# Performance work log

Hardware: AMD Instinct MI355X
Metric: run time of the kernel (lower is better)

The kernel has to match this reference:

```python
import jax, jax.numpy as jnp
import numpy as np

K = 5        # kernel_size per pseudo-dim
DIM = 2      # pseudo-coordinate dimensionality
K2 = K * K   # total kernel weight matrices
N_NODES = 50000


def spline_basis(edge_attr):
    """Open B-spline basis, degree=1, dim=2. Returns basis [E,4], weight_index [E,4]."""
    v = edge_attr * (K - 1)                      # [E,2], pseudo in [0,1]
    lo = jnp.floor(v)
    frac = v - lo                                # [E,2]
    lo = lo.astype(jnp.int32)
    fac = jnp.stack([1.0 - frac, frac], axis=-1)                 # [E,2,2] (dim, bit)
    idx = jnp.clip(lo[..., None] + jnp.arange(2), 0, K - 1)      # [E,2,2]
    b0 = jnp.array([0, 1, 0, 1])  # bit for dim 0, per spline term
    b1 = jnp.array([0, 0, 1, 1])  # bit for dim 1
    basis = fac[:, 0, b0] * fac[:, 1, b1]        # [E,4]
    wi = idx[:, 0, b0] * K + idx[:, 1, b1]       # [E,4] flat kernel index
    return basis, wi


def spline_conv(x, src, dst, basis, wi, W, root, bias, n_nodes):
    """SplineConv with mean aggregation, root weight and bias.
    x:[N,Fin] W:[K2,Fin,Fout] root:[Fin,Fout] bias:[Fout]"""
    E = src.shape[0]
    K2_, Fin, Fout = W.shape
    # scatter the 4 sparse basis values into a dense per-edge kernel-coeff matrix [E,K2]
    coeff = jnp.zeros((E, K2_), x.dtype).at[jnp.arange(E)[:, None], wi].add(basis)
    xj = x[src]                                  # gather source features [E,Fin]
    msg = jnp.zeros((E, Fout), x.dtype)
    for k in range(K2_):                         # fixed small loop over 25 kernels
        msg = msg + coeff[:, k:k + 1] * (xj @ W[k])
    agg = jax.ops.segment_sum(msg, dst, num_segments=n_nodes)    # [N,Fout]
    deg = jax.ops.segment_sum(jnp.ones((E,), x.dtype), dst, num_segments=n_nodes)
    agg = agg / jnp.clip(deg, 1.0)[:, None]      # mean aggregation
    return agg + x @ root + bias


def setup_inputs() -> dict:
    key = jax.random.key(0)
    ks = jax.random.split(key, 9)
    E = 800000
    Fin, H, C = 64, 16, 7
    x = jax.random.normal(ks[0], (N_NODES, Fin), dtype=jnp.float32)
    edge_index = jax.random.randint(ks[1], (2, E), 0, N_NODES, dtype=jnp.int64)
    edge_attr = jax.random.uniform(ks[2], (E, DIM), dtype=jnp.float32)
    s1 = 1.0 / np.sqrt(Fin)
    s2 = 1.0 / np.sqrt(H)
    W1 = jax.random.uniform(ks[3], (K2, Fin, H), jnp.float32, -s1, s1)
    root1 = jax.random.uniform(ks[4], (Fin, H), jnp.float32, -s1, s1)
    bias1 = jax.random.uniform(ks[5], (H,), jnp.float32, -s1, s1)
    W2 = jax.random.uniform(ks[6], (K2, H, C), jnp.float32, -s2, s2)
    root2 = jax.random.uniform(ks[7], (H, C), jnp.float32, -s2, s2)
    bias2 = jax.random.uniform(ks[8], (C,), jnp.float32, -s2, s2)
    return {"x": x, "edge_index": edge_index, "edge_attr": edge_attr,
            "W1": W1, "root1": root1, "bias1": bias1,
            "W2": W2, "root2": root2, "bias2": bias2}


def reference(x, edge_index, edge_attr, W1, root1, bias1, W2, root2, bias2):
    src = edge_index[0]
    dst = edge_index[1]
    basis, wi = spline_basis(edge_attr)
    h = jax.nn.relu(spline_conv(x, src, dst, basis, wi, W1, root1, bias1, N_NODES))
    # dropout(p=0.6) is identity in eval mode
    out = spline_conv(h, src, dst, basis, wi, W2, root2, bias2, N_NODES)
    return jax.nn.log_softmax(out, axis=1)
```

## Files before the change

kernel.cpp:

```cpp
#include <hip/hip_runtime.h>

#define KK2 25
#define FIN 64
#define HH 16
#define CC 7

#define SCAN_VPT 4
#define SCAN_BLK 256
#define SCAN_CHUNK (SCAN_VPT * SCAN_BLK)

__device__ inline unsigned short f2bf(float f) {
    unsigned u = __float_as_uint(f);
    return (unsigned short)((u + 0x7FFFu + ((u >> 16) & 1u)) >> 16);
}
__device__ inline float bf2f(unsigned short b) {
    return __uint_as_float(((unsigned)b) << 16);
}

__global__ void k_hist(const int* __restrict__ ei, int* __restrict__ cnt, int E) {
    int e = blockIdx.x * 256 + threadIdx.x;
    if (e < E) atomicAdd(&cnt[ei[E + e]], 1);
}

__global__ void k_bsum(const int* __restrict__ cnt, int* __restrict__ bsum, int N) {
    int b = blockIdx.x, t = threadIdx.x;
    int base = b * SCAN_CHUNK + t * SCAN_VPT;
    int s = 0;
#pragma unroll
    for (int j = 0; j < SCAN_VPT; j++) {
        int i = base + j;
        if (i < N) s += cnt[i];
    }
#pragma unroll
    for (int d = 1; d < 64; d <<= 1) s += __shfl_xor(s, d, 64);
    __shared__ int sd[SCAN_BLK / 64];
    if ((t & 63) == 0) sd[t >> 6] = s;
    __syncthreads();
    if (t == 0) {
        int tot = 0;
        for (int w = 0; w < SCAN_BLK / 64; w++) tot += sd[w];
        bsum[b] = tot;
    }
}

__global__ void k_bscan(const int* __restrict__ bsum, int* __restrict__ boff, int nblk) {
    int t = threadIdx.x;
    __shared__ int sd[256];
    int v = (t < nblk) ? bsum[t] : 0;
    sd[t] = v;
    __syncthreads();
    for (int off = 1; off < 256; off <<= 1) {
        int u = (t >= off) ? sd[t - off] : 0;
        __syncthreads();
        sd[t] += u;
        __syncthreads();
    }
    boff[t] = sd[t] - v;
}

__global__ void k_sfin(const int* __restrict__ cnt, const int* __restrict__ boff,
                       int* __restrict__ rowStart, int* __restrict__ cursor, int N) {
    int b = blockIdx.x, t = threadIdx.x;
    int base = b * SCAN_CHUNK + t * SCAN_VPT;
    int v[SCAN_VPT];
    int s = 0;
#pragma unroll
    for (int j = 0; j < SCAN_VPT; j++) {
        int i = base + j;
        v[j] = (i < N) ? cnt[i] : 0;
        s += v[j];
    }
    __shared__ int sd[SCAN_BLK];
    sd[t] = s;
    __syncthreads();
    for (int off = 1; off < SCAN_BLK; off <<= 1) {
        int u = (t >= off) ? sd[t - off] : 0;
        __syncthreads();
        sd[t] += u;
        __syncthreads();
    }
    int run = sd[t] - s + boff[b];
#pragma unroll
    for (int j = 0; j < SCAN_VPT; j++) {
        int i = base + j;
        if (i < N) {
            rowStart[i] = run;
            cursor[i] = run;
            run += v[j];
            if (i == N - 1) rowStart[N] = run;
        }
    }
}

__global__ void k_scatter(const float* __restrict__ attr, const int* __restrict__ ei,
                          int* __restrict__ cursor, float4* __restrict__ rec, int E) {
    int e = blockIdx.x * 256 + threadIdx.x;
    if (e >= E) return;
    float v0 = attr[2 * e] * 4.0f, v1 = attr[2 * e + 1] * 4.0f;
    float l0 = floorf(v0), l1 = floorf(v1);
    float f0 = v0 - l0, f1 = v1 - l1;
    int i0 = (int)l0, i1 = (int)l1;
    int i0a = min(max(i0, 0), 4), i0b = min(max(i0 + 1, 0), 4);
    int i1a = min(max(i1, 0), 4), i1b = min(max(i1 + 1, 0), 4);
    float4 b;
    b.x = (1.0f - f0) * (1.0f - f1);
    b.y = f0 * (1.0f - f1);
    b.z = (1.0f - f0) * f1;
    b.w = f0 * f1;
    unsigned pack = (unsigned)(i0a * 5 + i1a) | ((unsigned)(i0b * 5 + i1a) << 8) |
                    ((unsigned)(i0a * 5 + i1b) << 16) | ((unsigned)(i0b * 5 + i1b) << 24);
    int s = ei[e], d = ei[E + e];
    int pos = atomicAdd(&cursor[d], 1);
    rec[2 * pos] = b;
    rec[2 * pos + 1] = make_float4(__int_as_float(s), __uint_as_float(pack), 0.0f, 0.0f);
}

__global__ void k_prepW(const float* __restrict__ W1, const float* __restrict__ W2,
                        float* __restrict__ B1t, float* __restrict__ W2p) {
    int tid = blockIdx.x * 256 + threadIdx.x;
    if (tid < KK2 * FIN * HH) {
        int c = tid >> 6, i = tid & 63;
        int k = c >> 4, h = c & 15;
        B1t[tid] = W1[(k * FIN + i) * HH + h];
    }
    if (tid < KK2 * HH * CC) {
        int k = tid / (HH * CC), r = tid % (HH * CC);
        int i = r / CC, c = r % CC;
        W2p[(k * HH + i) * 8 + c] = W2[tid];
    }
}

__global__ void k_y1(const float* __restrict__ x, const float* __restrict__ B1t,
                     unsigned short* __restrict__ y1Tb, int N, int nbl, int nwpx) {
    int xcd = blockIdx.x & 7;
    int idx = blockIdx.x >> 3;
    int k = idx / nwpx;
    int nw = idx % nwpx;
    int nwin = xcd * nwpx + nw;
    if (nwin >= nbl) return;
    int n = nwin * 256 + threadIdx.x;
    if (n >= N) return;
    float4 xr[16];
    const float4* xp = (const float4*)(x + (size_t)n * 64);
#pragma unroll
    for (int i = 0; i < 16; i++) xr[i] = xp[i];
    const float* B = B1t + k * 16 * 64;
    float acc[16];
#pragma unroll
    for (int h4 = 0; h4 < 4; h4++) {
        float a0 = 0, a1 = 0, a2 = 0, a3 = 0;
        const float4* b0 = (const float4*)(B + (h4 * 4 + 0) * 64);
        const float4* b1 = (const float4*)(B + (h4 * 4 + 1) * 64);
        const float4* b2 = (const float4*)(B + (h4 * 4 + 2) * 64);
        const float4* b3 = (const float4*)(B + (h4 * 4 + 3) * 64);
#pragma unroll
        for (int i = 0; i < 16; i++) {
            float4 xi = xr[i];
            float4 v0 = b0[i], v1 = b1[i], v2 = b2[i], v3 = b3[i];
            a0 += xi.x * v0.x + xi.y * v0.y + xi.z * v0.z + xi.w * v0.w;
            a1 += xi.x * v1.x + xi.y * v1.y + xi.z * v1.z + xi.w * v1.w;
            a2 += xi.x * v2.x + xi.y * v2.y + xi.z * v2.z + xi.w * v2.w;
            a3 += xi.x * v3.x + xi.y * v3.y + xi.z * v3.z + xi.w * v3.w;
        }
        acc[h4 * 4 + 0] = a0; acc[h4 * 4 + 1] = a1;
        acc[h4 * 4 + 2] = a2; acc[h4 * 4 + 3] = a3;
    }
    uint4 p0, p1;
    unsigned* pw = (unsigned*)&p0;
#pragma unroll
    for (int j = 0; j < 8; j++)
        ((unsigned*)&p0)[j < 4 ? j : j] = 0;
    unsigned tmp[8];
#pragma unroll
    for (int j = 0; j < 8; j++)
        tmp[j] = (unsigned)f2bf(acc[2 * j]) | ((unsigned)f2bf(acc[2 * j + 1]) << 16);
    p0 = make_uint4(tmp[0], tmp[1], tmp[2], tmp[3]);
    p1 = make_uint4(tmp[4], tmp[5], tmp[6], tmp[7]);
    (void)pw;
    uint4* yo = (uint4*)(y1Tb + ((size_t)k * N + n) * 16);
    yo[0] = p0;
    yo[1] = p1;
}

__global__ void k_agg1(const int* __restrict__ rowStart, const float4* __restrict__ rec,
                       const unsigned short* __restrict__ y1Tb, float* __restrict__ agg1,
                       int N) {
    int n = blockIdx.x * 4 + (threadIdx.x >> 6);
    if (n >= N) return;
    int lane = threadIdx.x & 63;
    int sub = lane >> 4, h = lane & 15;
    int start = rowStart[n], end = rowStart[n + 1];
    float acc = 0.0f;
    size_t NN = (size_t)N;
    for (int i = start + sub; i < end; i += 4) {
        float4 b = rec[2 * i];
        float4 meta = rec[2 * i + 1];
        int s = __float_as_int(meta.x);
        unsigned w = __float_as_uint(meta.y);
        acc += b.x * bf2f(y1Tb[((w & 255u) * NN + s) * 16 + h]);
        acc += b.y * bf2f(y1Tb[(((w >> 8) & 255u) * NN + s) * 16 + h]);
        acc += b.z * bf2f(y1Tb[(((w >> 16) & 255u) * NN + s) * 16 + h]);
        acc += b.w * bf2f(y1Tb[((w >> 24) * NN + s) * 16 + h]);
    }
    acc += __shfl_xor(acc, 16, 64);
    acc += __shfl_xor(acc, 32, 64);
    if (lane < 16) agg1[(size_t)n * 16 + h] = acc;
}

__global__ void k_upd1(const float* __restrict__ x, const float* __restrict__ agg1,
                       const int* __restrict__ rowStart, const float* __restrict__ root1,
                       const float* __restrict__ bias1, const float* __restrict__ W2p,
                       float* __restrict__ h1, unsigned short* __restrict__ y2Tb, int N) {
    int n = blockIdx.x * 256 + threadIdx.x;
    if (n >= N) return;
    float inv = 1.0f / (float)max(rowStart[n + 1] - rowStart[n], 1);
    float r[16];
#pragma unroll
    for (int h = 0; h < 16; h++) r[h] = agg1[(size_t)n * 16 + h] * inv + bias1[h];
    const float* xrow = x + (size_t)n * 64;
    for (int i = 0; i < 64; i++) {
        float xi = xrow[i];
        const float* rr = root1 + i * 16;
#pragma unroll
        for (int h = 0; h < 16; h++) r[h] += xi * rr[h];
    }
#pragma unroll
    for (int h = 0; h < 16; h++) r[h] = fmaxf(r[h], 0.0f);
    float4* ho = (float4*)(h1 + (size_t)n * 16);
#pragma unroll
    for (int j = 0; j < 4; j++) ho[j] = make_float4(r[4*j], r[4*j+1], r[4*j+2], r[4*j+3]);
    for (int k = 0; k < 25; k++) {
        float z[8] = {0, 0, 0, 0, 0, 0, 0, 0};
        const float4* wp = (const float4*)(W2p + k * 128);
#pragma unroll
        for (int i = 0; i < 16; i++) {
            float hi = r[i];
            float4 lo = wp[2 * i], hv = wp[2 * i + 1];
            z[0] += hi * lo.x; z[1] += hi * lo.y; z[2] += hi * lo.z; z[3] += hi * lo.w;
            z[4] += hi * hv.x; z[5] += hi * hv.y; z[6] += hi * hv.z; z[7] += hi * hv.w;
        }
        uint4 p;
        p.x = (unsigned)f2bf(z[0]) | ((unsigned)f2bf(z[1]) << 16);
        p.y = (unsigned)f2bf(z[2]) | ((unsigned)f2bf(z[3]) << 16);
        p.z = (unsigned)f2bf(z[4]) | ((unsigned)f2bf(z[5]) << 16);
        p.w = (unsigned)f2bf(z[6]) | ((unsigned)f2bf(z[7]) << 16);
        *(uint4*)(y2Tb + ((size_t)k * N + n) * 8) = p;
    }
}

__global__ void k_agg2(const int* __restrict__ rowStart, const float4* __restrict__ rec,
                       const unsigned short* __restrict__ y2Tb, float* __restrict__ agg2,
                       int N) {
    int n = blockIdx.x * 4 + (threadIdx.x >> 6);
    if (n >= N) return;
    int lane = threadIdx.x & 63;
    int sub = lane >> 3, c = lane & 7;
    int start = rowStart[n], end = rowStart[n + 1];
    float acc = 0.0f;
    size_t NN = (size_t)N;
    for (int i = start + sub; i < end; i += 8) {
        float4 b = rec[2 * i];
        float4 meta = rec[2 * i + 1];
        int s = __float_as_int(meta.x);
        unsigned w = __float_as_uint(meta.y);
        acc += b.x * bf2f(y2Tb[((w & 255u) * NN + s) * 8 + c]);
        acc += b.y * bf2f(y2Tb[(((w >> 8) & 255u) * NN + s) * 8 + c]);
        acc += b.z * bf2f(y2Tb[(((w >> 16) & 255u) * NN + s) * 8 + c]);
        acc += b.w * bf2f(y2Tb[((w >> 24) * NN + s) * 8 + c]);
    }
    acc += __shfl_xor(acc, 8, 64);
    acc += __shfl_xor(acc, 16, 64);
    acc += __shfl_xor(acc, 32, 64);
    if (lane < 8) agg2[(size_t)n * 8 + c] = acc;
}

__global__ void k_fin2(const float* __restrict__ h1, const float* __restrict__ agg2,
                       const int* __restrict__ rowStart, const float* __restrict__ root2,
                       const float* __restrict__ bias2, float* __restrict__ out, int N) {
    int n = blockIdx.x * 256 + threadIdx.x;
    if (n >= N) return;
    float inv = 1.0f / (float)max(rowStart[n + 1] - rowStart[n], 1);
    float z[7];
#pragma unroll
    for (int c = 0; c < 7; c++) z[c] = agg2[(size_t)n * 8 + c] * inv + bias2[c];
    const float* hrow = h1 + (size_t)n * 16;
#pragma unroll
    for (int i = 0; i < 16; i++) {
        float hi = hrow[i];
        const float* rr = root2 + i * 7;
#pragma unroll
        for (int c = 0; c < 7; c++) z[c] += hi * rr[c];
    }
    float m = z[0];
#pragma unroll
    for (int c = 1; c < 7; c++) m = fmaxf(m, z[c]);
    float ssum = 0.0f;
#pragma unroll
    for (int c = 0; c < 7; c++) ssum += expf(z[c] - m);
    float ls = logf(ssum);
    float* orow = out + (size_t)n * 7;
#pragma unroll
    for (int c = 0; c < 7; c++) orow[c] = z[c] - m - ls;
}

extern "C" void kernel_launch(void* const* d_in, const int* in_sizes, int n_in,
                              void* d_out, int out_size, void* d_ws, size_t ws_size,
                              hipStream_t stream) {
    const float* x     = (const float*)d_in[0];
    const int*   ei    = (const int*)d_in[1];
    const float* attr  = (const float*)d_in[2];
    const float* W1    = (const float*)d_in[3];
    const float* root1 = (const float*)d_in[4];
    const float* bias1 = (const float*)d_in[5];
    const float* W2    = (const float*)d_in[6];
    const float* root2 = (const float*)d_in[7];
    const float* bias2 = (const float*)d_in[8];
    float* out = (float*)d_out;

    int N = in_sizes[0] / FIN;
    int E = in_sizes[1] / 2;

    char* w = (char*)d_ws;
    size_t off = 0;
    auto alloc = [&](size_t bytes) -> void* {
        void* p = w + off;
        off += (bytes + 255) & ~(size_t)255;
        return p;
    };
    int*      cnt      = (int*)alloc((size_t)N * 4);
    int*      rowStart = (int*)alloc((size_t)(N + 1) * 4);
    int*      cursor   = (int*)alloc((size_t)N * 4);
    int*      bsum     = (int*)alloc(260 * 4);
    int*      boff     = (int*)alloc(260 * 4);
    float4*   rec      = (float4*)alloc((size_t)E * 32);
    float*    agg1     = (float*)alloc((size_t)N * 64);
    float*    h1       = (float*)alloc((size_t)N * 64);
    float*    agg2     = (float*)alloc((size_t)N * 32);
    float*    B1t      = (float*)alloc((size_t)KK2 * FIN * HH * 4);
    float*    W2p      = (float*)alloc((size_t)KK2 * HH * 8 * 4);
    unsigned short* y1Tb = (unsigned short*)alloc((size_t)N * 400 * 2);
    unsigned short* y2Tb = y1Tb;
    (void)ws_size; (void)n_in; (void)out_size;

    hipMemsetAsync(cnt, 0, (size_t)N * 4, stream);

    int ebl = (E + 255) / 256;
    int nbl = (N + 255) / 256;
    int sblk = (N + SCAN_CHUNK - 1) / SCAN_CHUNK;
    int nwpx = (nbl + 7) / 8;

    k_hist<<<ebl, 256, 0, stream>>>(ei, cnt, E);
    k_bsum<<<sblk, SCAN_BLK, 0, stream>>>(cnt, bsum, N);
    k_bscan<<<1, 256, 0, stream>>>(bsum, boff, sblk);
    k_sfin<<<sblk, SCAN_BLK, 0, stream>>>(cnt, boff, rowStart, cursor, N);
    k_scatter<<<ebl, 256, 0, stream>>>(attr, ei, cursor, rec, E);
    k_prepW<<<(KK2 * FIN * HH + 255) / 256, 256, 0, stream>>>(W1, W2, B1t, W2p);
    k_y1<<<8 * KK2 * nwpx, 256, 0, stream>>>(x, B1t, y1Tb, N, nbl, nwpx);
    k_agg1<<<(N + 3) / 4, 256, 0, stream>>>(rowStart, rec, y1Tb, agg1, N);
    k_upd1<<<nbl, 256, 0, stream>>>(x, agg1, rowStart, root1, bias1, W2p, h1, y2Tb, N);
    k_agg2<<<(N + 3) / 4, 256, 0, stream>>>(rowStart, rec, y2Tb, agg2, N);
    k_fin2<<<nbl, 256, 0, stream>>>(h1, agg2, rowStart, root2, bias2, out, N);
}
```

Measured before the change: 357.0 us.

## Reuse x rows across five kernel matrices and coalesce y1 stores via LDS

k_y1 now has each block load its 256 x rows once and compute five kernel-weight products instead of one, cutting redundant x reads by a factor of five. Each wave stages its bf16 outputs in padded shared memory and writes them back as contiguous uint4 stores, replacing the 32-byte per-thread strided writes. The XCD-aware block mapping is dropped. The grid shrinks to 5*nbl blocks, which reduces parallelism, and two block-wide barriers are added per k iteration.

```diff
diff --git a/kernel.cpp b/kernel.cpp
--- a/kernel.cpp
+++ b/kernel.cpp
@@ -4,6 +4,7 @@
 #define FIN 64
 #define HH 16
 #define CC 7
+#define KSPLIT 5
 
 #define SCAN_VPT 4
 #define SCAN_BLK 256
@@ -131,55 +132,60 @@
 }
 
 __global__ void k_y1(const float* __restrict__ x, const float* __restrict__ B1t,
-                     unsigned short* __restrict__ y1Tb, int N, int nbl, int nwpx) {
-    int xcd = blockIdx.x & 7;
-    int idx = blockIdx.x >> 3;
-    int k = idx / nwpx;
-    int nw = idx % nwpx;
-    int nwin = xcd * nwpx + nw;
-    if (nwin >= nbl) return;
+                     unsigned short* __restrict__ y1Tb, int N, int nbl) {
+    __shared__ uint4 sh[4][144];
+    int kg = blockIdx.x / nbl;
+    int nwin = blockIdx.x % nbl;
     int n = nwin * 256 + threadIdx.x;
-    if (n >= N) return;
+    int wv = threadIdx.x >> 6, lane = threadIdx.x & 63;
+    bool active = (n < N);
     float4 xr[16];
-    const float4* xp = (const float4*)(x + (size_t)n * 64);
-#pragma unroll
-    for (int i = 0; i < 16; i++) xr[i] = xp[i];
-    const float* B = B1t + k * 16 * 64;
-    float acc[16];
-#pragma unroll
-    for (int h4 = 0; h4 < 4; h4++) {
-        float a0 = 0, a1 = 0, a2 = 0, a3 = 0;
-        const float4* b0 = (const float4*)(B + (h4 * 4 + 0) * 64);
-        const float4* b1 = (const float4*)(B + (h4 * 4 + 1) * 64);
-        const float4* b2 = (const float4*)(B + (h4 * 4 + 2) * 64);
-        const float4* b3 = (const float4*)(B + (h4 * 4 + 3) * 64);
-#pragma unroll
-        for (int i = 0; i < 16; i++) {
-            float4 xi = xr[i];
-            float4 v0 = b0[i], v1 = b1[i], v2 = b2[i], v3 = b3[i];
-            a0 += xi.x * v0.x + xi.y * v0.y + xi.z * v0.z + xi.w * v0.w;
-            a1 += xi.x * v1.x + xi.y * v1.y + xi.z * v1.z + xi.w * v1.w;
-            a2 += xi.x * v2.x + xi.y * v2.y + xi.z * v2.z + xi.w * v2.w;
-            a3 += xi.x * v3.x + xi.y * v3.y + xi.z * v3.z + xi.w * v3.w;
+    if (active) {
+        const float4* xp = (const float4*)(x + (size_t)n * 64);
+#pragma unroll
+        for (int i = 0; i < 16; i++) xr[i] = xp[i];
+    }
+    int nwb = nwin * 256 + wv * 64;
+    int valid = min(64, max(0, N - nwb)) * 2;
+
+    for (int dk = 0; dk < KSPLIT; dk++) {
+        int k = kg * KSPLIT + dk;
+        const float* B = B1t + k * 16 * 64;
+        unsigned tmp[8];
+        if (active) {
+#pragma unroll
+            for (int h4 = 0; h4 < 4; h4++) {
+                float a0 = 0, a1 = 0, a2 = 0, a3 = 0;
+                const float4* b0 = (const float4*)(B + (h4 * 4 + 0) * 64);
+                const float4* b1 = (const float4*)(B + (h4 * 4 + 1) * 64);
+                const float4* b2 = (const float4*)(B + (h4 * 4 + 2) * 64);
+                const float4* b3 = (const float4*)(B + (h4 * 4 + 3) * 64);
+#pragma unroll
+                for (int i = 0; i < 16; i++) {
+                    float4 xi = xr[i];
+                    float4 v0 = b0[i], v1 = b1[i], v2 = b2[i], v3 = b3[i];
+                    a0 += xi.x * v0.x + xi.y * v0.y + xi.z * v0.z + xi.w * v0.w;
+                    a1 += xi.x * v1.x + xi.y * v1.y + xi.z * v1.z + xi.w * v1.w;
+                    a2 += xi.x * v2.x + xi.y * v2.y + xi.z * v2.z + xi.w * v2.w;
+                    a3 += xi.x * v3.x + xi.y * v3.y + xi.z * v3.z + xi.w * v3.w;
+                }
+                tmp[h4 * 2 + 0] = (unsigned)f2bf(a0) | ((unsigned)f2bf(a1) << 16);
+                tmp[h4 * 2 + 1] = (unsigned)f2bf(a2) | ((unsigned)f2bf(a3) << 16);
+            }
+        } else {
+#pragma unroll
+            for (int j = 0; j < 8; j++) tmp[j] = 0;
         }
-        acc[h4 * 4 + 0] = a0; acc[h4 * 4 + 1] = a1;
-        acc[h4 * 4 + 2] = a2; acc[h4 * 4 + 3] = a3;
-    }
-    uint4 p0, p1;
-    unsigned* pw = (unsigned*)&p0;
-#pragma unroll
-    for (int j = 0; j < 8; j++)
-        ((unsigned*)&p0)[j < 4 ? j : j] = 0;
-    unsigned tmp[8];
-#pragma unroll
-    for (int j = 0; j < 8; j++)
-        tmp[j] = (unsigned)f2bf(acc[2 * j]) | ((unsigned)f2bf(acc[2 * j + 1]) << 16);
-    p0 = make_uint4(tmp[0], tmp[1], tmp[2], tmp[3]);
-    p1 = make_uint4(tmp[4], tmp[5], tmp[6], tmp[7]);
-    (void)pw;
-    uint4* yo = (uint4*)(y1Tb + ((size_t)k * N + n) * 16);
-    yo[0] = p0;
-    yo[1] = p1;
+        int i0 = lane * 2, i1 = lane * 2 + 1;
+        sh[wv][i0 + (i0 >> 3)] = make_uint4(tmp[0], tmp[1], tmp[2], tmp[3]);
+        sh[wv][i1 + (i1 >> 3)] = make_uint4(tmp[4], tmp[5], tmp[6], tmp[7]);
+        __syncthreads();
+        uint4* gbase = (uint4*)(y1Tb + ((size_t)k * N + nwb) * 16);
+        int j0 = lane, j1 = lane + 64;
+        if (j0 < valid) gbase[j0] = sh[wv][j0 + (j0 >> 3)];
+        if (j1 < valid) gbase[j1] = sh[wv][j1 + (j1 >> 3)];
+        __syncthreads();
+    }
 }
 
 __global__ void k_agg1(const int* __restrict__ rowStart, const float4* __restrict__ rec,
@@ -347,7 +353,6 @@
     int ebl = (E + 255) / 256;
     int nbl = (N + 255) / 256;
     int sblk = (N + SCAN_CHUNK - 1) / SCAN_CHUNK;
-    int nwpx = (nbl + 7) / 8;
 
     k_hist<<<ebl, 256, 0, stream>>>(ei, cnt, E);
     k_bsum<<<sblk, SCAN_BLK, 0, stream>>>(cnt, bsum, N);
@@ -355,7 +360,7 @@
     k_sfin<<<sblk, SCAN_BLK, 0, stream>>>(cnt, boff, rowStart, cursor, N);
     k_scatter<<<ebl, 256, 0, stream>>>(attr, ei, cursor, rec, E);
     k_prepW<<<(KK2 * FIN * HH + 255) / 256, 256, 0, stream>>>(W1, W2, B1t, W2p);
-    k_y1<<<8 * KK2 * nwpx, 256, 0, stream>>>(x, B1t, y1Tb, N, nbl, nwpx);
+    k_y1<<<KSPLIT * nbl, 256, 0, stream>>>(x, B1t, y1Tb, N, nbl);
     k_agg1<<<(N + 3) / 4, 256, 0, stream>>>(rowStart, rec, y1Tb, agg1, N);
     k_upd1<<<nbl, 256, 0, stream>>>(x, agg1, rowStart, root1, bias1, W2p, h1, y2Tb, N);
     k_agg2<<<(N + 3) / 4, 256, 0, stream>>>(rowStart, rec, y2Tb, agg2, N);
```

New measurement: 310.0 us. 13.2% less time.
